# Kernel optimization log

Hardware: AMD Instinct MI355X
Metric: run time of the kernel (lower is better)

Reference implementation:

```python
import jax, jax.numpy as jnp
import numpy as np

N_NODES = 100000
N_EDGES = 3200000
IN_CH = 256
OUT_CH = 128


def setup_inputs() -> dict:
    key = jax.random.key(0)
    k1, k2, k3, k4, k5 = jax.random.split(key, 5)
    x = jax.random.normal(k1, (N_NODES, IN_CH), dtype=jnp.float32)
    edge_src = jax.random.randint(k2, (N_EDGES,), 0, N_NODES, dtype=jnp.int64 if jax.config.jax_enable_x64 else jnp.int32)
    edge_dst = jax.random.randint(k3, (N_EDGES,), 0, N_NODES, dtype=jnp.int64 if jax.config.jax_enable_x64 else jnp.int32)
    edge_vals = jax.random.uniform(k4, (N_EDGES,), dtype=jnp.float32)
    weight = jax.random.normal(k5, (IN_CH, OUT_CH), dtype=jnp.float32) * (2.0 / (IN_CH + OUT_CH)) ** 0.5  # glorot
    bias = jnp.zeros((OUT_CH,), dtype=jnp.float32)
    return {"x": x, "edge_src": edge_src, "edge_dst": edge_dst,
            "edge_vals": edge_vals, "weight": weight, "bias": bias}


def reference(x, edge_src, edge_dst, edge_vals, weight, bias):
    # out = A @ (x @ W) + b, with A given in COO form (edge_src=row, edge_dst=col, edge_vals)
    xw = x @ weight                                  # [N, out]
    msgs = xw[edge_dst] * edge_vals[:, None]         # gather source features, scale by edge weight
    agg = jax.ops.segment_sum(msgs, edge_src, num_segments=N_NODES)  # scatter-add to rows
    return agg + bias
```

## Files before the change

### kernel.cpp

```cpp
#include <hip/hip_runtime.h>

#define N_NODES 100000
#define N_EDGES 3200000
#define IN_CH   256
#define OUT_CH  128

#define BSH        5
#define BN         32
#define NBIN       3125
#define NBLK1      392
#define EPB1       8192
#define NS1        (NBIN * NBLK1)
#define SCAN_CHUNK 8192
#define NBLK_S1    ((NS1 + SCAN_CHUNK - 1) / SCAN_CHUNK)
#define SCAP       2048

#define OFF_XWB    0
#define OFF_WBF    25600000
#define OFF_CNTT   25665536
#define OFF_CNTA   30565536
#define OFF_RPA    35465536
#define OFF_RPT    40365552
#define OFF_BS     45265552
#define OFF_RPN    45266576
#define OFF_PACKED 45666592

typedef __attribute__((ext_vector_type(8))) short    bf8;
typedef __attribute__((ext_vector_type(4))) float    f4;
typedef __attribute__((ext_vector_type(4))) unsigned uv4;

__device__ __forceinline__ unsigned f2bf(float f) {
    unsigned u = __float_as_uint(f);
    return (u + 0x7fffu + ((u >> 16) & 1u)) >> 16;
}

__global__ __launch_bounds__(256) void wcvt_kernel(const float* __restrict__ w,
                                                   unsigned short* __restrict__ wbf) {
    int t = threadIdx.x;
    int k = blockIdx.x * 2 + (t >> 7);
    int n = t & 127;
    wbf[n * 256 + k] = (unsigned short)f2bf(w[k * 128 + n]);
}

__global__ __launch_bounds__(256) void gemm_kernel(const float* __restrict__ x,
                                                   const unsigned short* __restrict__ wbf,
                                                   unsigned* __restrict__ xwb) {
    int wave = threadIdx.x >> 6;
    int lane = threadIdx.x & 63;
    int m = lane & 15;
    int q = lane >> 4;
    int r0 = blockIdx.x * 64 + wave * 16;

    int arow = r0 + m;
    if (arow >= N_NODES) arow = N_NODES - 1;
    const float* xr = x + (long long)arow * IN_CH + q * 8;

    f4 acc[8];
#pragma unroll
    for (int ct = 0; ct < 8; ++ct) acc[ct] = (f4){0.f, 0.f, 0.f, 0.f};

#pragma unroll
    for (int ks = 0; ks < 8; ++ks) {
        float4 xa = *(const float4*)(xr + ks * 32);
        float4 xb = *(const float4*)(xr + ks * 32 + 4);
        bf8 a;
        a[0] = (short)f2bf(xa.x); a[1] = (short)f2bf(xa.y);
        a[2] = (short)f2bf(xa.z); a[3] = (short)f2bf(xa.w);
        a[4] = (short)f2bf(xb.x); a[5] = (short)f2bf(xb.y);
        a[6] = (short)f2bf(xb.z); a[7] = (short)f2bf(xb.w);
#pragma unroll
        for (int ct = 0; ct < 8; ++ct) {
            uv4 u = *(const uv4*)&wbf[(ct * 16 + m) * 256 + ks * 32 + q * 8];
            bf8 b = __builtin_bit_cast(bf8, u);
            acc[ct] = __builtin_amdgcn_mfma_f32_16x16x32_bf16(a, b, acc[ct], 0, 0, 0);
        }
    }

#pragma unroll
    for (int ct = 0; ct < 8; ++ct) {
#pragma unroll
        for (int r = 0; r < 4; ++r) {
            float v = acc[ct][r];
            float p = __shfl_xor(v, 1, 64);
            unsigned mine = f2bf(v), oth = f2bf(p);
            if (!(m & 1)) {
                int row = r0 + q * 4 + r;
                if (row < N_NODES)
                    xwb[row * 64 + ct * 8 + (m >> 1)] = mine | (oth << 16);
            }
        }
    }
}

__global__ __launch_bounds__(1024) void h1_kernel(const int* __restrict__ src,
                                                  int* __restrict__ cntT) {
    __shared__ int lc[NBIN];
    int tid = threadIdx.x;
    for (int i = tid; i < NBIN; i += 1024) lc[i] = 0;
    __syncthreads();
#pragma unroll
    for (int k = 0; k < EPB1 / 4096; ++k) {
        int i = blockIdx.x * EPB1 + k * 4096 + tid * 4;
        if (i < N_EDGES) {
            int4 s = *(const int4*)&src[i];
            atomicAdd(&lc[s.x >> BSH], 1);
            atomicAdd(&lc[s.y >> BSH], 1);
            atomicAdd(&lc[s.z >> BSH], 1);
            atomicAdd(&lc[s.w >> BSH], 1);
        }
    }
    __syncthreads();
    for (int i = tid; i < NBIN; i += 1024)
        cntT[blockIdx.x * NBIN + i] = lc[i];
}

__global__ __launch_bounds__(256) void transpose_kernel(const int* __restrict__ in,
                                                        int* __restrict__ out,
                                                        int R, int C) {
    __shared__ int t[32][33];
    int tx = threadIdx.x & 31, ty0 = threadIdx.x >> 5;
    int c0 = blockIdx.x * 32, r0 = blockIdx.y * 32;
#pragma unroll
    for (int i = 0; i < 4; ++i) {
        int r = r0 + ty0 + i * 8, c = c0 + tx;
        t[ty0 + i * 8][tx] = (r < R && c < C) ? in[r * C + c] : 0;
    }
    __syncthreads();
#pragma unroll
    for (int i = 0; i < 4; ++i) {
        int c = c0 + ty0 + i * 8, r = r0 + tx;
        if (c < C && r < R) out[c * R + r] = t[tx][ty0 + i * 8];
    }
}

__global__ __launch_bounds__(256) void scan_s1(const int* __restrict__ cnt,
                                               int* __restrict__ bsum) {
    __shared__ int wsum[4];
    int tid = threadIdx.x, lane = tid & 63, wid = tid >> 6;
    int acc = 0;
#pragma unroll
    for (int k = 0; k < SCAN_CHUNK / 1024; ++k) {
        int i0 = blockIdx.x * SCAN_CHUNK + k * 1024 + tid * 4;
        if (i0 < NS1) {
            int4 v = *(const int4*)&cnt[i0];
            acc += v.x + v.y + v.z + v.w;
        }
    }
#pragma unroll
    for (int off = 32; off; off >>= 1) acc += __shfl_down(acc, off, 64);
    if (lane == 0) wsum[wid] = acc;
    __syncthreads();
    if (tid == 0) bsum[blockIdx.x] = wsum[0] + wsum[1] + wsum[2] + wsum[3];
}

__global__ __launch_bounds__(256) void scan_s2(int* __restrict__ bsum,
                                               int* __restrict__ rpA,
                                               int* __restrict__ rpn) {
    __shared__ int wsum[4];
    int tid = threadIdx.x, lane = tid & 63, wid = tid >> 6;
    int v = (tid < NBLK_S1) ? bsum[tid] : 0;
    int s = v;
#pragma unroll
    for (int off = 1; off < 64; off <<= 1) {
        int t = __shfl_up(s, off, 64);
        if (lane >= off) s += t;
    }
    if (lane == 63) wsum[wid] = s;
    __syncthreads();
    int w0 = wsum[0], w1 = wsum[1], w2 = wsum[2], w3 = wsum[3];
    int woff = (wid > 0 ? w0 : 0) + (wid > 1 ? w1 : 0) + (wid > 2 ? w2 : 0);
    if (tid < NBLK_S1) bsum[tid] = woff + s - v;
    if (tid == 0) {
        int tot = w0 + w1 + w2 + w3;
        rpA[NS1] = tot;
        rpn[N_NODES] = tot;
    }
}

__global__ __launch_bounds__(256) void scan_s3(const int* __restrict__ cnt,
                                               const int* __restrict__ bsum,
                                               int* __restrict__ rpA) {
    __shared__ int wsum[4];
    int tid = threadIdx.x, lane = tid & 63, wid = tid >> 6;
    int carry = bsum[blockIdx.x];
#pragma unroll
    for (int k = 0; k < SCAN_CHUNK / 1024; ++k) {
        int i0 = blockIdx.x * SCAN_CHUNK + k * 1024 + tid * 4;
        int4 v = make_int4(0, 0, 0, 0);
        if (i0 < NS1) v = *(const int4*)&cnt[i0];
        int sum4 = v.x + v.y + v.z + v.w;
        int s = sum4;
#pragma unroll
        for (int off = 1; off < 64; off <<= 1) {
            int t = __shfl_up(s, off, 64);
            if (lane >= off) s += t;
        }
        if (lane == 63) wsum[wid] = s;
        __syncthreads();
        int w0 = wsum[0], w1 = wsum[1], w2 = wsum[2], w3 = wsum[3];
        int woff = (wid > 0 ? w0 : 0) + (wid > 1 ? w1 : 0) + (wid > 2 ? w2 : 0);
        int excl = carry + woff + (s - sum4);
        if (i0 < NS1)
            *(int4*)&rpA[i0] = make_int4(excl, excl + v.x, excl + v.x + v.y,
                                         excl + v.x + v.y + v.z);
        carry += w0 + w1 + w2 + w3;
        __syncthreads();
    }
}

__global__ __launch_bounds__(1024) void b1_kernel(const int* __restrict__ src,
                                                  const int* __restrict__ dst,
                                                  const float* __restrict__ val,
                                                  const int* __restrict__ rpT,
                                                  int2* __restrict__ p1) {
    __shared__ int lcur[NBIN];
    int tid = threadIdx.x;
    for (int i = tid; i < NBIN; i += 1024)
        lcur[i] = rpT[blockIdx.x * NBIN + i];
    __syncthreads();
#pragma unroll
    for (int k = 0; k < EPB1 / 4096; ++k) {
        int i = blockIdx.x * EPB1 + k * 4096 + tid * 4;
        if (i < N_EDGES) {
            int4   s = *(const int4*)&src[i];
            int4   d = *(const int4*)&dst[i];
            float4 v = *(const float4*)&val[i];
            int p;
            p = atomicAdd(&lcur[s.x >> BSH], 1);
            p1[p] = make_int2(d.x | ((s.x & (BN - 1)) << 17), __float_as_int(v.x));
            p = atomicAdd(&lcur[s.y >> BSH], 1);
            p1[p] = make_int2(d.y | ((s.y & (BN - 1)) << 17), __float_as_int(v.y));
            p = atomicAdd(&lcur[s.z >> BSH], 1);
            p1[p] = make_int2(d.z | ((s.z & (BN - 1)) << 17), __float_as_int(v.z));
            p = atomicAdd(&lcur[s.w >> BSH], 1);
            p1[p] = make_int2(d.w | ((s.w & (BN - 1)) << 17), __float_as_int(v.w));
        }
    }
}

__global__ __launch_bounds__(256) void sortf_kernel(const int2* __restrict__ p1,
                                                    const int* __restrict__ rpA,
                                                    int2* __restrict__ packed,
                                                    int* __restrict__ rpn) {
    __shared__ int  lcnt[BN];
    __shared__ int  lcur[BN];
    __shared__ int2 sbuf[SCAP];
    int b = blockIdx.x, tid = threadIdx.x;
    int beg = rpA[b * NBLK1];
    int end = rpA[(b + 1) * NBLK1];
    int n = end - beg;

    if (tid < BN) lcnt[tid] = 0;
    __syncthreads();

    if (n <= SCAP) {
        for (int e = tid; e < n; e += 256) {
            int2 q = p1[beg + e];
            sbuf[e] = q;
            atomicAdd(&lcnt[(q.x >> 17) & (BN - 1)], 1);
        }
    } else {
        for (int e = beg + tid; e < end; e += 256)
            atomicAdd(&lcnt[(p1[e].x >> 17) & (BN - 1)], 1);
    }
    __syncthreads();

    if (tid < BN) {
        int c = lcnt[tid];
        int v = c;
#pragma unroll
        for (int off = 1; off < BN; off <<= 1) {
            int t = __shfl_up(v, off, 64);
            if (tid >= off) v += t;
        }
        int excl = beg + v - c;
        lcur[tid] = excl;
        rpn[b * BN + tid] = excl;
    }
    __syncthreads();

    if (n <= SCAP) {
        for (int e = tid; e < n; e += 256) {
            int2 q = sbuf[e];
            int p = atomicAdd(&lcur[(q.x >> 17) & (BN - 1)], 1);
            packed[p] = make_int2(q.x & 0x1FFFF, q.y);
        }
    } else {
        for (int e = beg + tid; e < end; e += 256) {
            int2 q = p1[e];
            int p = atomicAdd(&lcur[(q.x >> 17) & (BN - 1)], 1);
            packed[p] = make_int2(q.x & 0x1FFFF, q.y);
        }
    }
}

__global__ __launch_bounds__(256) void aggregate_kernel(const int* __restrict__ rp,
                                                        const int2* __restrict__ packed,
                                                        const unsigned* __restrict__ xwb,
                                                        const float* __restrict__ bias,
                                                        float* __restrict__ out) {
    int node = blockIdx.x * 4 + (threadIdx.x >> 6);
    int lane = threadIdx.x & 63;
    float2 acc = *(const float2*)&bias[lane * 2];

    int beg = rp[node];
    int end = rp[node + 1];
    for (int t = beg; t < end; t += 64) {
        int2 rec = make_int2(0, 0);
        if (t + lane < end) rec = packed[t + lane];
        int cnt = end - t; if (cnt > 64) cnt = 64;
        int cnt8 = (cnt + 7) & ~7;
        for (int j = 0; j < cnt8; j += 8) {
            unsigned u[8]; float vv[8];
#pragma unroll
            for (int k = 0; k < 8; ++k) {
                int d  = __builtin_amdgcn_readlane(rec.x, j + k);
                int vb = __builtin_amdgcn_readlane(rec.y, j + k);
                vv[k] = __int_as_float(vb);
                u[k]  = xwb[d * 64 + lane];
            }
#pragma unroll
            for (int k = 0; k < 8; ++k) {
                acc.x += vv[k] * __uint_as_float(u[k] << 16);
                acc.y += vv[k] * __uint_as_float(u[k] & 0xffff0000u);
            }
        }
    }
    *(float2*)&out[(long long)node * OUT_CH + lane * 2] = acc;
}

extern "C" void kernel_launch(void* const* d_in, const int* in_sizes, int n_in,
                              void* d_out, int out_size, void* d_ws, size_t ws_size,
                              hipStream_t stream) {
    const float* x     = (const float*)d_in[0];
    const int*   esrc  = (const int*)d_in[1];
    const int*   edst  = (const int*)d_in[2];
    const float* evals = (const float*)d_in[3];
    const float* w     = (const float*)d_in[4];
    const float* bias  = (const float*)d_in[5];
    float* out = (float*)d_out;

    char* ws = (char*)d_ws;
    unsigned*       xwb    = (unsigned*)      (ws + OFF_XWB);
    unsigned short* wbf    = (unsigned short*)(ws + OFF_WBF);
    int*            cntT   = (int*)           (ws + OFF_CNTT);
    int*            cntA   = (int*)           (ws + OFF_CNTA);
    int*            rpA    = (int*)           (ws + OFF_RPA);
    int*            rpT    = (int*)           (ws + OFF_RPT);
    int*            bsum   = (int*)           (ws + OFF_BS);
    int*            rpn    = (int*)           (ws + OFF_RPN);
    int2*           packed = (int2*)          (ws + OFF_PACKED);
    int2*           p1     = (int2*)          d_out;

    wcvt_kernel<<<128, 256, 0, stream>>>(w, wbf);
    gemm_kernel<<<(N_NODES + 63) / 64, 256, 0, stream>>>(x, wbf, xwb);
    h1_kernel<<<NBLK1, 1024, 0, stream>>>(esrc, cntT);
    transpose_kernel<<<dim3((NBIN + 31) / 32, (NBLK1 + 31) / 32), 256, 0, stream>>>(
        cntT, cntA, NBLK1, NBIN);
    scan_s1<<<NBLK_S1, 256, 0, stream>>>(cntA, bsum);
    scan_s2<<<1, 256, 0, stream>>>(bsum, rpA, rpn);
    scan_s3<<<NBLK_S1, 256, 0, stream>>>(cntA, bsum, rpA);
    transpose_kernel<<<dim3((NBLK1 + 31) / 32, (NBIN + 31) / 32), 256, 0, stream>>>(
        rpA, rpT, NBIN, NBLK1);
    b1_kernel<<<NBLK1, 1024, 0, stream>>>(esrc, edst, evals, rpT, p1);
    sortf_kernel<<<NBIN, 256, 0, stream>>>(p1, rpA, packed, rpn);
    aggregate_kernel<<<N_NODES / 4, 256, 0, stream>>>(rpn, packed, xwb, bias, out);
}
```

Baseline: 430.0 us.

## Retune binning blocks, use packed bf16 convert, and widen aggregate gather batch

Cuts the number of histogram and binning blocks from 392 to 256, with 12500 edges per block, which shrinks the per-block count matrix and its scan and transpose work. In the GEMM, the hand-written bf16 rounding is replaced by the hardware v_cvt_pk_bf16_f32 instruction. The aggregate kernel now issues 16 independent gathers per batch instead of 8, and uses packed float2 vector FMAs to expose more memory-level parallelism. The larger gather batch raises register pressure and adds padding waste for low-degree nodes.

New measurement: 433.6 us. About the same (+0.8%).

```diff
diff --git a/kernel.cpp b/kernel.cpp
--- a/kernel.cpp
+++ b/kernel.cpp
@@ -8,8 +8,9 @@
 #define BSH        5
 #define BN         32
 #define NBIN       3125
-#define NBLK1      392
-#define EPB1       8192
+#define NBLK1      256
+#define EPB1       12500
+#define ITER1      4
 #define NS1        (NBIN * NBLK1)
 #define SCAN_CHUNK 8192
 #define NBLK_S1    ((NS1 + SCAN_CHUNK - 1) / SCAN_CHUNK)
@@ -18,20 +19,27 @@
 #define OFF_XWB    0
 #define OFF_WBF    25600000
 #define OFF_CNTT   25665536
-#define OFF_CNTA   30565536
-#define OFF_RPA    35465536
-#define OFF_RPT    40365552
-#define OFF_BS     45265552
-#define OFF_RPN    45266576
-#define OFF_PACKED 45666592
+#define OFF_CNTA   28865536
+#define OFF_RPA    32065536
+#define OFF_RPT    35265552
+#define OFF_BS     38465552
+#define OFF_RPN    38466576
+#define OFF_PACKED 38866592
 
 typedef __attribute__((ext_vector_type(8))) short    bf8;
 typedef __attribute__((ext_vector_type(4))) float    f4;
 typedef __attribute__((ext_vector_type(4))) unsigned uv4;
+typedef __attribute__((ext_vector_type(2))) float    f2v;
 
 __device__ __forceinline__ unsigned f2bf(float f) {
     unsigned u = __float_as_uint(f);
     return (u + 0x7fffu + ((u >> 16) & 1u)) >> 16;
+}
+
+__device__ __forceinline__ unsigned cvt_pk_bf16(float lo, float hi) {
+    unsigned r;
+    asm("v_cvt_pk_bf16_f32 %0, %1, %2" : "=v"(r) : "v"(lo), "v"(hi));
+    return r;
 }
 
 __global__ __launch_bounds__(256) void wcvt_kernel(const float* __restrict__ w,
@@ -63,11 +71,12 @@
     for (int ks = 0; ks < 8; ++ks) {
         float4 xa = *(const float4*)(xr + ks * 32);
         float4 xb = *(const float4*)(xr + ks * 32 + 4);
-        bf8 a;
-        a[0] = (short)f2bf(xa.x); a[1] = (short)f2bf(xa.y);
-        a[2] = (short)f2bf(xa.z); a[3] = (short)f2bf(xa.w);
-        a[4] = (short)f2bf(xb.x); a[5] = (short)f2bf(xb.y);
-        a[6] = (short)f2bf(xb.z); a[7] = (short)f2bf(xb.w);
+        uv4 au;
+        au[0] = cvt_pk_bf16(xa.x, xa.y);
+        au[1] = cvt_pk_bf16(xa.z, xa.w);
+        au[2] = cvt_pk_bf16(xb.x, xb.y);
+        au[3] = cvt_pk_bf16(xb.z, xb.w);
+        bf8 a = __builtin_bit_cast(bf8, au);
 #pragma unroll
         for (int ct = 0; ct < 8; ++ct) {
             uv4 u = *(const uv4*)&wbf[(ct * 16 + m) * 256 + ks * 32 + q * 8];
@@ -82,11 +91,11 @@
         for (int r = 0; r < 4; ++r) {
             float v = acc[ct][r];
             float p = __shfl_xor(v, 1, 64);
-            unsigned mine = f2bf(v), oth = f2bf(p);
+            unsigned wpk = cvt_pk_bf16(v, p);
             if (!(m & 1)) {
                 int row = r0 + q * 4 + r;
                 if (row < N_NODES)
-                    xwb[row * 64 + ct * 8 + (m >> 1)] = mine | (oth << 16);
+                    xwb[row * 64 + ct * 8 + (m >> 1)] = wpk;
             }
         }
     }
@@ -96,12 +105,13 @@
                                                   int* __restrict__ cntT) {
     __shared__ int lc[NBIN];
     int tid = threadIdx.x;
+    int bend = blockIdx.x * EPB1 + EPB1;
     for (int i = tid; i < NBIN; i += 1024) lc[i] = 0;
     __syncthreads();
 #pragma unroll
-    for (int k = 0; k < EPB1 / 4096; ++k) {
+    for (int k = 0; k < ITER1; ++k) {
         int i = blockIdx.x * EPB1 + k * 4096 + tid * 4;
-        if (i < N_EDGES) {
+        if (i < bend) {
             int4 s = *(const int4*)&src[i];
             atomicAdd(&lc[s.x >> BSH], 1);
             atomicAdd(&lc[s.y >> BSH], 1);
@@ -215,13 +225,14 @@
                                                   int2* __restrict__ p1) {
     __shared__ int lcur[NBIN];
     int tid = threadIdx.x;
+    int bend = blockIdx.x * EPB1 + EPB1;
     for (int i = tid; i < NBIN; i += 1024)
         lcur[i] = rpT[blockIdx.x * NBIN + i];
     __syncthreads();
 #pragma unroll
-    for (int k = 0; k < EPB1 / 4096; ++k) {
+    for (int k = 0; k < ITER1; ++k) {
         int i = blockIdx.x * EPB1 + k * 4096 + tid * 4;
-        if (i < N_EDGES) {
+        if (i < bend) {
             int4   s = *(const int4*)&src[i];
             int4   d = *(const int4*)&dst[i];
             float4 v = *(const float4*)&val[i];
@@ -301,7 +312,9 @@
                                                         float* __restrict__ out) {
     int node = blockIdx.x * 4 + (threadIdx.x >> 6);
     int lane = threadIdx.x & 63;
-    float2 acc = *(const float2*)&bias[lane * 2];
+    float2 bb = *(const float2*)&bias[lane * 2];
+    f2v acc; acc[0] = bb.x; acc[1] = bb.y;
+    const unsigned* xl = xwb + lane;
 
     int beg = rp[node];
     int end = rp[node + 1];
@@ -309,24 +322,26 @@
         int2 rec = make_int2(0, 0);
         if (t + lane < end) rec = packed[t + lane];
         int cnt = end - t; if (cnt > 64) cnt = 64;
-        int cnt8 = (cnt + 7) & ~7;
-        for (int j = 0; j < cnt8; j += 8) {
-            unsigned u[8]; float vv[8];
-#pragma unroll
-            for (int k = 0; k < 8; ++k) {
+        int cntB = (cnt + 15) & ~15;
+        for (int j = 0; j < cntB; j += 16) {
+            unsigned u[16]; float vv[16];
+#pragma unroll
+            for (int k = 0; k < 16; ++k) {
                 int d  = __builtin_amdgcn_readlane(rec.x, j + k);
-                int vb = __builtin_amdgcn_readlane(rec.y, j + k);
-                vv[k] = __int_as_float(vb);
-                u[k]  = xwb[d * 64 + lane];
+                vv[k]  = __int_as_float(__builtin_amdgcn_readlane(rec.y, j + k));
+                u[k]   = xl[d * 64];
             }
 #pragma unroll
-            for (int k = 0; k < 8; ++k) {
-                acc.x += vv[k] * __uint_as_float(u[k] << 16);
-                acc.y += vv[k] * __uint_as_float(u[k] & 0xffff0000u);
+            for (int k = 0; k < 16; ++k) {
+                f2v bvec;
+                bvec[0] = __uint_as_float(u[k] << 16);
+                bvec[1] = __uint_as_float(u[k] & 0xffff0000u);
+                acc += vv[k] * bvec;
             }
         }
     }
-    *(float2*)&out[(long long)node * OUT_CH + lane * 2] = acc;
+    float2 o; o.x = acc[0]; o.y = acc[1];
+    *(float2*)&out[(long long)node * OUT_CH + lane * 2] = o;
 }
 
 extern "C" void kernel_launch(void* const* d_in, const int* in_sizes, int n_in,
```
